# Kernel tuning notes

Hardware: AMD Instinct MI355X
Metric: run time of the kernel (lower is better)

Reference implementation:

```python
import jax, jax.numpy as jnp
import numpy as np

HEADS = 4; C = 128; D = C // HEADS; L = 2
TKG_LEN = 24; NU = 2000; NL = 5000; E = 40000
B = 64; S = 128; MAX_USER = 5000; MAX_LOC = 10000


def _seg_softmax(logits, seg, num_seg):
    # per-destination-node softmax over incoming edges, per head. logits: [E, H]
    m = jax.ops.segment_max(logits, seg, num_segments=num_seg)
    e = jnp.exp(logits - m[seg])
    z = jax.ops.segment_sum(e, seg, num_segments=num_seg)
    return e / (z[seg] + 1e-16)


def _hgt_layer(xu, xl, src_ul, dst_ul, src_lu, dst_lu, wu, bu, wl, bl, ra, rm, rp, skip):
    # PyG HGTConv math. wu/wl: [4,C,C] (k,q,v,a), bu/bl: [4,C];
    # ra/rm: [2,H,D,D] per edge type (0: user->loc, 1: loc->user); rp: [2,H]; skip: [2] (user, loc)
    def kqv(x, w, b):
        return [(x @ w[i] + b[i]).reshape(-1, HEADS, D) for i in range(3)]
    ku, qu, vu = kqv(xu, wu, bu)
    kl, ql, vl = kqv(xl, wl, bl)
    scale = 1.0 / np.sqrt(D).astype(np.float32)

    def edge_msg(k_src, v_src, q_dst, src, dst, a_rel, m_rel, p_rel, n_dst):
        kr = jnp.einsum('nhd,hde->nhe', k_src, a_rel)   # relation-transformed keys
        mr = jnp.einsum('nhd,hde->nhe', v_src, m_rel)   # relation-transformed messages
        logits = (q_dst[dst] * kr[src]).sum(-1) * p_rel * scale  # [E, H]
        alpha = _seg_softmax(logits, dst, n_dst)
        return jax.ops.segment_sum(mr[src] * alpha[..., None], dst, num_segments=n_dst)  # [N,H,D]

    agg_l = edge_msg(ku, vu, ql, src_ul, dst_ul, ra[0], rm[0], rp[0], xl.shape[0])
    agg_u = edge_msg(kl, vl, qu, src_lu, dst_lu, ra[1], rm[1], rp[1], xu.shape[0])

    def update(agg, x, wa, ba, s):
        out = jax.nn.gelu(agg.reshape(-1, C), approximate=False) @ wa + ba
        g = jax.nn.sigmoid(s)
        return g * out + (1.0 - g) * x

    return (update(agg_u, xu, wu[3], bu[3], skip[0]),
            update(agg_l, xl, wl[3], bl[3], skip[1]))


def setup_inputs():
    key = jax.random.key(0)
    ks = jax.random.split(key, 20)
    w = lambda k, shape, s=0.05: jax.random.normal(k, shape, jnp.float32) * s
    user_emb = w(ks[0], (MAX_USER, C), 0.1).at[0].set(0.0)  # padding_idx=0
    loc_emb = w(ks[1], (MAX_LOC, C), 0.1).at[0].set(0.0)
    return dict(
        user_emb=user_emb, loc_emb=loc_emb,
        lin_user_w=w(ks[2], (C, C)), lin_user_b=jnp.zeros((C,), jnp.float32),
        lin_loc_w=w(ks[3], (C, C)), lin_loc_b=jnp.zeros((C,), jnp.float32),
        w_user=w(ks[4], (L, 4, C, C)), b_user=jnp.zeros((L, 4, C), jnp.float32),
        w_loc=w(ks[5], (L, 4, C, C)), b_loc=jnp.zeros((L, 4, C), jnp.float32),
        rel_a=w(ks[6], (L, 2, HEADS, D, D), 1.0 / np.sqrt(D)),
        rel_m=w(ks[7], (L, 2, HEADS, D, D), 1.0 / np.sqrt(D)),
        rel_p=jnp.ones((L, 2, HEADS), jnp.float32),
        skip=jnp.ones((L, 2), jnp.float32),
        lin2_w=w(ks[8], (C, C)), lin2_b=jnp.zeros((C,), jnp.float32),
        user_ids=jax.random.randint(ks[9], (TKG_LEN, NU), 0, MAX_USER),
        loc_ids=jax.random.randint(ks[10], (TKG_LEN, NL), 0, MAX_LOC),
        ei_ul_src=jax.random.randint(ks[11], (TKG_LEN, E), 0, NU),
        ei_ul_dst=jax.random.randint(ks[12], (TKG_LEN, E), 0, NL),
        ei_lu_src=jax.random.randint(ks[13], (TKG_LEN, E), 0, NL),
        ei_lu_dst=jax.random.randint(ks[14], (TKG_LEN, E), 0, NU),
        traj=jax.random.randint(ks[15], (B, S), 0, NL),
        tkg_idx=jax.random.randint(ks[16], (B, S), 0, TKG_LEN),
    )


def reference(user_emb, loc_emb, lin_user_w, lin_user_b, lin_loc_w, lin_loc_b,
              w_user, b_user, w_loc, b_loc, rel_a, rel_m, rel_p, skip,
              lin2_w, lin2_b, user_ids, loc_ids, ei_ul_src, ei_ul_dst,
              ei_lu_src, ei_lu_dst, traj, tkg_idx):
    def encode(uid, lid, sul, dul, slu, dlu):
        # EmbeddingLayer lookup + AggregationLayer: per-node-type Linear + relu, HGT convs, lin2 on locations
        xu = jax.nn.relu(user_emb[uid] @ lin_user_w + lin_user_b)
        xl = jax.nn.relu(loc_emb[lid] @ lin_loc_w + lin_loc_b)
        for i in range(L):
            xu, xl = _hgt_layer(xu, xl, sul, dul, slu, dlu,
                                w_user[i], b_user[i], w_loc[i], b_loc[i],
                                rel_a[i], rel_m[i], rel_p[i], skip[i])
        return xl @ lin2_w + lin2_b

    # the torch loop over tkg_dl snapshots -> vmap over the tkg_len axis
    tkg_out = jax.vmap(encode)(user_ids, loc_ids, ei_ul_src, ei_ul_dst, ei_lu_src, ei_lu_dst)
    # tkg_filter: one-hot mask multiply-sum == direct gather tkg_out[tkg_idx[b,s], traj[b,s]]
    tkg_traj = tkg_out[tkg_idx, traj]  # [B, S, C]
    return (tkg_traj, tkg_out)
```

## Files before the change

kernel.cpp:

```cpp
#include <hip/hip_runtime.h>
#include <math.h>

#define T_LEN 24
#define NUU 2000
#define NLL 5000
#define NE 40000
#define CH 128
#define NH 4
#define HD 32
#define TCHUNK 8

typedef __attribute__((ext_vector_type(8))) short short8;
typedef __attribute__((ext_vector_type(4))) float f32x4;

static inline int cdiv(int a, int b) { return (a + b - 1) / b; }

__device__ __forceinline__ unsigned short f2bf(float x) {
    unsigned u = __float_as_uint(x);
    unsigned r = (u + 0x7fff + ((u >> 16) & 1)) >> 16;
    return (unsigned short)r;
}
__device__ __forceinline__ float bf2f(unsigned short h) {
    return __uint_as_float(((unsigned)h) << 16);
}
__device__ __forceinline__ float2 bf2x(unsigned u) {
    float2 r;
    r.x = __uint_as_float(u << 16);
    r.y = __uint_as_float(u & 0xffff0000u);
    return r;
}

__global__ void fill_zero_int(int* __restrict__ p, int n) {
    int i = blockIdx.x * blockDim.x + threadIdx.x;
    if (i < n) p[i] = 0;
}

__global__ void histo_kernel(const int* __restrict__ dst, int* __restrict__ deg, int n) {
    int idx = blockIdx.x * blockDim.x + threadIdx.x;
    if (idx >= T_LEN * NE) return;
    int t = idx / NE;
    atomicAdd(&deg[t * n + dst[idx]], 1);
}

__global__ __launch_bounds__(256) void scan_off(const int* __restrict__ deg, int* __restrict__ offo, int n) {
    __shared__ int part[256];
    int t = blockIdx.x, tid = threadIdx.x;
    int items = (n + 255) / 256;
    int start = tid * items, end = min(start + items, n);
    const int* dt = deg + t * n;
    int s = 0;
    for (int i = start; i < end; ++i) s += dt[i];
    part[tid] = s;
    __syncthreads();
    for (int d = 1; d < 256; d <<= 1) {
        int v = (tid >= d) ? part[tid - d] : 0;
        __syncthreads();
        part[tid] += v;
        __syncthreads();
    }
    int run = part[tid] - s;
    int* ot = offo + t * (n + 1);
    if (tid == 0) ot[0] = 0;
    for (int i = start; i < end; ++i) { run += dt[i]; ot[i + 1] = run; }
}

__global__ void copy_cur(const int* __restrict__ offo, int* __restrict__ cur, int n) {
    int idx = blockIdx.x * blockDim.x + threadIdx.x;
    if (idx >= T_LEN * n) return;
    int t = idx / n, i = idx - t * n;
    cur[idx] = offo[t * (n + 1) + i];
}

__global__ void scatter_perm(const int* __restrict__ dst, int* __restrict__ cur,
                             int* __restrict__ perm, int n) {
    int idx = blockIdx.x * blockDim.x + threadIdx.x;
    if (idx >= T_LEN * NE) return;
    int t = idx / NE, e = idx - t * NE;
    int d = dst[idx];
    int pos = atomicAdd(&cur[t * n + d], 1);
    perm[t * NE + pos] = e;
}

__global__ void src_sorted_k(const int* __restrict__ src, const int* __restrict__ perm,
                             int* __restrict__ out) {
    int idx = blockIdx.x * blockDim.x + threadIdx.x;
    if (idx >= T_LEN * NE) return;
    int t = idx / NE;
    out[idx] = src[(size_t)t * NE + perm[idx]];
}

__global__ __launch_bounds__(256) void build_fused(
    const float* __restrict__ w, const float* __restrict__ b,
    const float* __restrict__ ra, const float* __restrict__ rm,
    float* __restrict__ Wf, float* __restrict__ bf) {
    int idx = blockIdx.x * 256 + threadIdx.x;
    if (idx >= 128 * 384) return;
    int c = idx / 384, col = idx - c * 384;
    if (col < 128) {
        Wf[c * 384 + col] = w[16384 + c * 128 + col];
        if (c == 0) bf[col] = b[128 + col];
    } else {
        int sec = (col - 128) >> 7;
        int hc = (col - 128) & 127;
        int h = hc >> 5, e2 = hc & 31;
        const float* A = (sec == 0 ? ra : rm) + h * 1024;
        const float* wsrc = w + (sec == 0 ? 0 : 2) * 16384;
        const float* bsrc = b + (sec == 0 ? 0 : 2) * 128;
        float s = 0.f, sb = 0.f;
#pragma unroll
        for (int d = 0; d < 32; ++d) {
            float a = A[d * 32 + e2];
            s += wsrc[c * 128 + h * 32 + d] * a;
            sb += bsrc[h * 32 + d] * a;
        }
        Wf[c * 384 + col] = s;
        if (c == 0) bf[col] = sb;
    }
}

__global__ void bprep_kernel(const float* __restrict__ W, unsigned short* __restrict__ prep, int N) {
    int idx = blockIdx.x * blockDim.x + threadIdx.x;
    if (idx >= 128 * N) return;
    int k = idx / N, n = idx - k * N;
    float v = W[idx];
    unsigned short hi = f2bf(v);
    unsigned short lo = f2bf(v - bf2f(hi));
    int nt = n >> 6, nl = n & 63;
    size_t base = (size_t)nt * 16384 + (size_t)nl * 128 + k;
    prep[base] = hi;
    prep[base + 8192] = lo;
}

template <bool GATHER, int EPI>
__global__ __launch_bounds__(256) void gemm_mfma(
    const float* __restrict__ A, const int* __restrict__ ids,
    const unsigned short* __restrict__ prep, const float* __restrict__ bias,
    float* __restrict__ C, const float* __restrict__ Xold,
    const float* __restrict__ skipPtr, unsigned short* __restrict__ km,
    int M, int NC) {
    __shared__ __align__(16) char smem[65536];

    const int tid = threadIdx.x;
    const int lane = tid & 63;
    const int wid = tid >> 6;
    const int wm = wid >> 1, wn = wid & 1;
    const int m0 = blockIdx.x * 128;
    const int n0 = blockIdx.y * 64;
    const int l15 = lane & 15, l4 = lane >> 4;

    const unsigned short* bp = prep + (size_t)blockIdx.y * 16384;
    short8 bh[2][4], bl[2][4];
#pragma unroll
    for (int nf = 0; nf < 2; ++nf) {
        int ncol = wn * 32 + nf * 16 + l15;
#pragma unroll
        for (int ks = 0; ks < 4; ++ks) {
            size_t off = (size_t)ncol * 128 + ks * 32 + l4 * 8;
            bh[nf][ks] = *(const short8*)(bp + off);
            bl[nf][ks] = *(const short8*)(bp + 8192 + off);
        }
    }

#pragma unroll
    for (int i = 0; i < 16; ++i) {
        int flat = i * 256 + tid;
        int r = flat >> 5, c4 = flat & 31;
        int gr = m0 + r;
        if (gr >= M) gr = M - 1;
        int arow = GATHER ? ids[gr] : gr;
        float4 v = *(const float4*)(A + (size_t)arow * 128 + c4 * 4);
        unsigned short h0 = f2bf(v.x), h1 = f2bf(v.y), h2 = f2bf(v.z), h3 = f2bf(v.w);
        unsigned short q0 = f2bf(v.x - bf2f(h0)), q1 = f2bf(v.y - bf2f(h1));
        unsigned short q2 = f2bf(v.z - bf2f(h2)), q3 = f2bf(v.w - bf2f(h3));
        uint2 hp, lp;
        hp.x = (unsigned)h0 | ((unsigned)h1 << 16);
        hp.y = (unsigned)h2 | ((unsigned)h3 << 16);
        lp.x = (unsigned)q0 | ((unsigned)q1 << 16);
        lp.y = (unsigned)q2 | ((unsigned)q3 << 16);
        int off = r * 256 + ((c4 * 8) ^ ((r & 7) << 4));
        *(uint2*)(smem + off) = hp;
        *(uint2*)(smem + 32768 + off) = lp;
    }
    __syncthreads();

    f32x4 acc[4][2];
#pragma unroll
    for (int m = 0; m < 4; ++m)
#pragma unroll
        for (int nf = 0; nf < 2; ++nf) acc[m][nf] = (f32x4)0.f;

#pragma unroll
    for (int ks = 0; ks < 4; ++ks) {
        short8 ah[4], al[4];
#pragma unroll
        for (int m = 0; m < 4; ++m) {
            int row = wm * 64 + m * 16 + l15;
            int off = row * 256 + ((ks * 64 + l4 * 16) ^ ((row & 7) << 4));
            ah[m] = *(const short8*)(smem + off);
            al[m] = *(const short8*)(smem + 32768 + off);
        }
#pragma unroll
        for (int m = 0; m < 4; ++m)
#pragma unroll
            for (int nf = 0; nf < 2; ++nf) {
                acc[m][nf] = __builtin_amdgcn_mfma_f32_16x16x32_bf16(al[m], bh[nf][ks], acc[m][nf], 0, 0, 0);
                acc[m][nf] = __builtin_amdgcn_mfma_f32_16x16x32_bf16(ah[m], bl[nf][ks], acc[m][nf], 0, 0, 0);
                acc[m][nf] = __builtin_amdgcn_mfma_f32_16x16x32_bf16(ah[m], bh[nf][ks], acc[m][nf], 0, 0, 0);
            }
    }

    float g = 0.f;
    if (EPI == 2) g = 1.f / (1.f + expf(-skipPtr[0]));
    float bias_v[2];
#pragma unroll
    for (int nf = 0; nf < 2; ++nf) bias_v[nf] = bias[n0 + wn * 32 + nf * 16 + l15];

#pragma unroll
    for (int m = 0; m < 4; ++m) {
#pragma unroll
        for (int nf = 0; nf < 2; ++nf) {
            int gc = n0 + wn * 32 + nf * 16 + l15;
#pragma unroll
            for (int i = 0; i < 4; ++i) {
                int gr = m0 + wm * 64 + m * 16 + l4 * 4 + i;
                if (gr >= M) continue;
                float x = acc[m][nf][i] + bias_v[nf];
                if (EPI == 1) x = fmaxf(x, 0.f);
                if (EPI == 2) {
                    float xo = Xold[(size_t)gr * NC + gc];
                    x = g * x + (1.f - g) * xo;
                }
                if (EPI == 3) {
                    if (gc < 128) C[(size_t)gr * 128 + gc] = x;
                    else km[(size_t)gr * 256 + (gc - 128)] = f2bf(x);
                } else {
                    C[(size_t)gr * NC + gc] = x;
                }
            }
        }
    }
}

__global__ __launch_bounds__(256) void agg_edges(
    const float* __restrict__ qD,
    const unsigned short* __restrict__ kmS,
    const int* __restrict__ off,
    const int* __restrict__ ssrc,
    const float* __restrict__ relp,
    float* __restrict__ agg,
    int nDst, int nSrc, int tBase) {
    int idx = blockIdx.x * 256 + threadIdx.x;
    int total = TCHUNK * nDst * NH * 4;
    if (idx >= total) return;
    int h = idx & 3;
    int slot = (idx >> 2) & 3;
    int node = (idx >> 4) % nDst;
    int tl = (idx >> 4) / nDst;
    int t = tBase + tl;

    size_t drow = (size_t)(tl * nDst + node);
    float p = relp[h] * 0.17677669529663687f;

    const float4* qp = (const float4*)(qD + drow * 128 + h * HD);
    float qr[HD];
#pragma unroll
    for (int j = 0; j < 8; j++) {
        float4 v = qp[j];
        qr[4 * j + 0] = v.x * p; qr[4 * j + 1] = v.y * p;
        qr[4 * j + 2] = v.z * p; qr[4 * j + 3] = v.w * p;
    }

    float m = -INFINITY, z = 0.f;
    float acc[HD];
#pragma unroll
    for (int d = 0; d < HD; d++) acc[d] = 0.f;

    int e0 = off[t * (nDst + 1) + node], e1 = off[t * (nDst + 1) + node + 1];
    const int* ssT = ssrc + (size_t)t * NE;

    for (int i = e0 + slot; i < e1; i += 4) {
        int s = ssT[i];
        const uint4* kp = (const uint4*)(kmS + ((size_t)(tl * nSrc + s)) * 256);
        uint ku[16], mu_[16];
        *(uint4*)(ku + 0) = kp[h * 4 + 0];
        *(uint4*)(ku + 4) = kp[h * 4 + 1];
        *(uint4*)(ku + 8) = kp[h * 4 + 2];
        *(uint4*)(ku + 12) = kp[h * 4 + 3];
        *(uint4*)(mu_ + 0) = kp[16 + h * 4 + 0];
        *(uint4*)(mu_ + 4) = kp[16 + h * 4 + 1];
        *(uint4*)(mu_ + 8) = kp[16 + h * 4 + 2];
        *(uint4*)(mu_ + 12) = kp[16 + h * 4 + 3];

        float dot = 0.f;
#pragma unroll
        for (int j = 0; j < 16; ++j) {
            float2 f = bf2x(ku[j]);
            dot = fmaf(qr[2 * j], f.x, dot);
            dot = fmaf(qr[2 * j + 1], f.y, dot);
        }
        float mn = fmaxf(m, dot);
        float c = __expf(m - mn);
        float w = __expf(dot - mn);
        z = z * c + w;
#pragma unroll
        for (int j = 0; j < 16; ++j) {
            float2 f = bf2x(mu_[j]);
            acc[2 * j] = fmaf(w, f.x, acc[2 * j] * c);
            acc[2 * j + 1] = fmaf(w, f.y, acc[2 * j + 1] * c);
        }
        m = mn;
    }

#pragma unroll
    for (int lm = 4; lm <= 8; lm <<= 1) {
        float mo = __shfl_xor(m, lm);
        float zo = __shfl_xor(z, lm);
        float mn = fmaxf(m, mo);
        float s1 = (m > -INFINITY) ? __expf(m - mn) : 0.f;
        float s2 = (mo > -INFINITY) ? __expf(mo - mn) : 0.f;
        z = z * s1 + zo * s2;
#pragma unroll
        for (int d = 0; d < HD; d++) {
            float ao = __shfl_xor(acc[d], lm);
            acc[d] = acc[d] * s1 + ao * s2;
        }
        m = mn;
    }

    if (slot == 0) {
        float inv = 1.f / (z + 1e-16f);
        float* op = agg + drow * CH + h * HD;
#pragma unroll
        for (int d = 0; d < HD; d++) {
            float v = acc[d] * inv;
            v = 0.5f * v * (1.f + erff(v * 0.70710678118654752f));
            op[d] = v;
        }
    }
}

__global__ void gather_traj(const float* __restrict__ tkg, const int* __restrict__ traj,
                            const int* __restrict__ tki, float* __restrict__ outp) {
    int idx = blockIdx.x * blockDim.x + threadIdx.x;
    if (idx >= 64 * 128 * 128) return;
    int r = idx >> 7, c2 = idx & 127;
    int t = tki[r], n = traj[r];
    outp[idx] = tkg[((size_t)t * NLL + n) * CH + c2];
}

extern "C" void kernel_launch(void* const* d_in, const int* in_sizes, int n_in,
                              void* d_out, int out_size, void* d_ws, size_t ws_size,
                              hipStream_t stream) {
    (void)in_sizes; (void)n_in; (void)out_size; (void)ws_size;
    const float* user_emb = (const float*)d_in[0];
    const float* loc_emb = (const float*)d_in[1];
    const float* lin_user_w = (const float*)d_in[2];
    const float* lin_user_b = (const float*)d_in[3];
    const float* lin_loc_w = (const float*)d_in[4];
    const float* lin_loc_b = (const float*)d_in[5];
    const float* w_user = (const float*)d_in[6];
    const float* b_user = (const float*)d_in[7];
    const float* w_loc = (const float*)d_in[8];
    const float* b_loc = (const float*)d_in[9];
    const float* rel_a = (const float*)d_in[10];
    const float* rel_m = (const float*)d_in[11];
    const float* rel_p = (const float*)d_in[12];
    const float* skip = (const float*)d_in[13];
    const float* lin2_w = (const float*)d_in[14];
    const float* lin2_b = (const float*)d_in[15];
    const int* user_ids = (const int*)d_in[16];
    const int* loc_ids = (const int*)d_in[17];
    const int* ei_ul_src = (const int*)d_in[18];
    const int* ei_ul_dst = (const int*)d_in[19];
    const int* ei_lu_src = (const int*)d_in[20];
    const int* ei_lu_dst = (const int*)d_in[21];
    const int* traj = (const int*)d_in[22];
    const int* tkg_idx = (const int*)d_in[23];
    float* outp = (float*)d_out;

    size_t woff = 0;
    char* base = (char*)d_ws;
    auto carve = [&](size_t bytes) -> void* {
        void* p = base + woff;
        woff += (bytes + 255) & ~(size_t)255;
        return p;
    };
    float* xu = (float*)carve((size_t)T_LEN * NUU * 128 * 4);
    float* xl = (float*)carve((size_t)T_LEN * NLL * 128 * 4);
    float* q_u = (float*)carve((size_t)TCHUNK * NUU * 128 * 4);
    float* q_l = (float*)carve((size_t)TCHUNK * NLL * 128 * 4);
    unsigned short* km_u = (unsigned short*)carve((size_t)TCHUNK * NUU * 256 * 2);
    unsigned short* km_l = (unsigned short*)carve((size_t)TCHUNK * NLL * 256 * 2);
    float* agg_u = (float*)carve((size_t)TCHUNK * NUU * 128 * 4);
    float* agg_l = (float*)carve((size_t)TCHUNK * NLL * 128 * 4);
    float* wf_u = (float*)carve(128 * 384 * 4);
    float* bf_u = (float*)carve(384 * 4);
    float* wf_l = (float*)carve(128 * 384 * 4);
    float* bf_l = (float*)carve(384 * 4);
    int* deg_ul = (int*)carve((size_t)T_LEN * NLL * 4);
    int* cur_ul = (int*)carve((size_t)T_LEN * NLL * 4);
    int* off_ul = (int*)carve((size_t)T_LEN * (NLL + 1) * 4);
    int* perm_ul = (int*)carve((size_t)T_LEN * NE * 4);
    int* ss_ul = (int*)carve((size_t)T_LEN * NE * 4);
    int* deg_lu = (int*)carve((size_t)T_LEN * NUU * 4);
    int* cur_lu = (int*)carve((size_t)T_LEN * NUU * 4);
    int* off_lu = (int*)carve((size_t)T_LEN * (NUU + 1) * 4);
    int* perm_lu = (int*)carve((size_t)T_LEN * NE * 4);
    int* ss_lu = (int*)carve((size_t)T_LEN * NE * 4);
    unsigned short* bp_lin_u = (unsigned short*)carve(128 * 512);
    unsigned short* bp_lin_l = (unsigned short*)carve(128 * 512);
    unsigned short* bp_lin2 = (unsigned short*)carve(128 * 512);
    unsigned short* bp_upd_u[2] = {(unsigned short*)carve(128 * 512), (unsigned short*)carve(128 * 512)};
    unsigned short* bp_upd_l[2] = {(unsigned short*)carve(128 * 512), (unsigned short*)carve(128 * 512)};
    unsigned short* bp_wf_u = (unsigned short*)carve(384 * 512);
    unsigned short* bp_wf_l = (unsigned short*)carve(384 * 512);

    fill_zero_int<<<cdiv(T_LEN * NLL, 256), 256, 0, stream>>>(deg_ul, T_LEN * NLL);
    fill_zero_int<<<cdiv(T_LEN * NUU, 256), 256, 0, stream>>>(deg_lu, T_LEN * NUU);
    histo_kernel<<<cdiv(T_LEN * NE, 256), 256, 0, stream>>>(ei_ul_dst, deg_ul, NLL);
    histo_kernel<<<cdiv(T_LEN * NE, 256), 256, 0, stream>>>(ei_lu_dst, deg_lu, NUU);
    scan_off<<<T_LEN, 256, 0, stream>>>(deg_ul, off_ul, NLL);
    scan_off<<<T_LEN, 256, 0, stream>>>(deg_lu, off_lu, NUU);
    copy_cur<<<cdiv(T_LEN * NLL, 256), 256, 0, stream>>>(off_ul, cur_ul, NLL);
    copy_cur<<<cdiv(T_LEN * NUU, 256), 256, 0, stream>>>(off_lu, cur_lu, NUU);
    scatter_perm<<<cdiv(T_LEN * NE, 256), 256, 0, stream>>>(ei_ul_dst, cur_ul, perm_ul, NLL);
    scatter_perm<<<cdiv(T_LEN * NE, 256), 256, 0, stream>>>(ei_lu_dst, cur_lu, perm_lu, NUU);
    src_sorted_k<<<cdiv(T_LEN * NE, 256), 256, 0, stream>>>(ei_ul_src, perm_ul, ss_ul);
    src_sorted_k<<<cdiv(T_LEN * NE, 256), 256, 0, stream>>>(ei_lu_src, perm_lu, ss_lu);

    bprep_kernel<<<64, 256, 0, stream>>>(lin_user_w, bp_lin_u, 128);
    bprep_kernel<<<64, 256, 0, stream>>>(lin_loc_w, bp_lin_l, 128);
    bprep_kernel<<<64, 256, 0, stream>>>(lin2_w, bp_lin2, 128);
    for (int l = 0; l < 2; ++l) {
        bprep_kernel<<<64, 256, 0, stream>>>(w_user + (size_t)(l * 4 + 3) * 16384, bp_upd_u[l], 128);
        bprep_kernel<<<64, 256, 0, stream>>>(w_loc + (size_t)(l * 4 + 3) * 16384, bp_upd_l[l], 128);
    }

    gemm_mfma<true, 1><<<dim3(cdiv(T_LEN * NUU, 128), 2), 256, 0, stream>>>(
        user_emb, user_ids, bp_lin_u, lin_user_b, xu, nullptr, nullptr, nullptr, T_LEN * NUU, 128);
    gemm_mfma<true, 1><<<dim3(cdiv(T_LEN * NLL, 128), 2), 256, 0, stream>>>(
        loc_emb, loc_ids, bp_lin_l, lin_loc_b, xl, nullptr, nullptr, nullptr, T_LEN * NLL, 128);

    for (int l = 0; l < 2; ++l) {
        build_fused<<<cdiv(128 * 384, 256), 256, 0, stream>>>(
            w_user + (size_t)l * 4 * 16384, b_user + l * 512,
            rel_a + (size_t)(l * 2 + 0) * 4096, rel_m + (size_t)(l * 2 + 0) * 4096, wf_u, bf_u);
        build_fused<<<cdiv(128 * 384, 256), 256, 0, stream>>>(
            w_loc + (size_t)l * 4 * 16384, b_loc + l * 512,
            rel_a + (size_t)(l * 2 + 1) * 4096, rel_m + (size_t)(l * 2 + 1) * 4096, wf_l, bf_l);
        bprep_kernel<<<192, 256, 0, stream>>>(wf_u, bp_wf_u, 384);
        bprep_kernel<<<192, 256, 0, stream>>>(wf_l, bp_wf_l, 384);

        for (int tb = 0; tb < T_LEN; tb += TCHUNK) {
            const int MU = TCHUNK * NUU;
            const int ML = TCHUNK * NLL;
            float* xu_c = xu + (size_t)tb * NUU * 128;
            float* xl_c = xl + (size_t)tb * NLL * 128;

            gemm_mfma<false, 3><<<dim3(cdiv(MU, 128), 6), 256, 0, stream>>>(
                xu_c, nullptr, bp_wf_u, bf_u, q_u, nullptr, nullptr, km_u, MU, 384);
            gemm_mfma<false, 3><<<dim3(cdiv(ML, 128), 6), 256, 0, stream>>>(
                xl_c, nullptr, bp_wf_l, bf_l, q_l, nullptr, nullptr, km_l, ML, 384);

            agg_edges<<<cdiv(TCHUNK * NLL * NH * 4, 256), 256, 0, stream>>>(
                q_l, km_u, off_ul, ss_ul, rel_p + (l * 2 + 0) * 4, agg_l, NLL, NUU, tb);
            agg_edges<<<cdiv(TCHUNK * NUU * NH * 4, 256), 256, 0, stream>>>(
                q_u, km_l, off_lu, ss_lu, rel_p + (l * 2 + 1) * 4, agg_u, NUU, NLL, tb);

            gemm_mfma<false, 2><<<dim3(cdiv(MU, 128), 2), 256, 0, stream>>>(
                agg_u, nullptr, bp_upd_u[l], b_user + l * 512 + 384,
                xu_c, xu_c, skip + l * 2 + 0, nullptr, MU, 128);
            gemm_mfma<false, 2><<<dim3(cdiv(ML, 128), 2), 256, 0, stream>>>(
                agg_l, nullptr, bp_upd_l[l], b_loc + l * 512 + 384,
                xl_c, xl_c, skip + l * 2 + 1, nullptr, ML, 128);
        }
    }

    float* tkg_out = outp + (size_t)64 * 128 * 128;
    gemm_mfma<false, 0><<<dim3(cdiv(T_LEN * NLL, 128), 2), 256, 0, stream>>>(
        xl, nullptr, bp_lin2, lin2_b, tkg_out, nullptr, nullptr, nullptr, T_LEN * NLL, 128);

    gather_traj<<<cdiv(64 * 128 * 128, 256), 256, 0, stream>>>(tkg_out, traj, tkg_idx, outp);
}
```

Measured before the change: 1.636 ms.

## Fuse CSR build kernels, remap GEMM workgroups per XCD, widen edge slots

Merges copy_cur into scan_off and fuses the scatter_perm and src_sorted kernels into one scatter_src that writes source ids straight into CSR order, which drops several launches and the perm buffers. The MFMA GEMM now remaps its flat workgroup id so that consecutive tiles land on the same XCD, aimed at better L2 locality across the chiplets. agg_edges uses 8 edge slots per (node, head) instead of 4, with one more shuffle-reduction step, to add parallelism for high-degree nodes. The cost is more threads doing reductions and extra integer math at GEMM entry; the order of edges within a segment is still nondeterministic.

```diff
diff --git a/kernel.cpp b/kernel.cpp
--- a/kernel.cpp
+++ b/kernel.cpp
@@ -42,7 +42,8 @@
     atomicAdd(&deg[t * n + dst[idx]], 1);
 }
 
-__global__ __launch_bounds__(256) void scan_off(const int* __restrict__ deg, int* __restrict__ offo, int n) {
+__global__ __launch_bounds__(256) void scan_off(const int* __restrict__ deg, int* __restrict__ offo,
+                                                int* __restrict__ cur, int n) {
     __shared__ int part[256];
     int t = blockIdx.x, tid = threadIdx.x;
     int items = (n + 255) / 256;
@@ -60,33 +61,23 @@
     }
     int run = part[tid] - s;
     int* ot = offo + t * (n + 1);
+    int* ct = cur + t * n;
     if (tid == 0) ot[0] = 0;
-    for (int i = start; i < end; ++i) { run += dt[i]; ot[i + 1] = run; }
-}
-
-__global__ void copy_cur(const int* __restrict__ offo, int* __restrict__ cur, int n) {
-    int idx = blockIdx.x * blockDim.x + threadIdx.x;
-    if (idx >= T_LEN * n) return;
-    int t = idx / n, i = idx - t * n;
-    cur[idx] = offo[t * (n + 1) + i];
-}
-
-__global__ void scatter_perm(const int* __restrict__ dst, int* __restrict__ cur,
-                             int* __restrict__ perm, int n) {
-    int idx = blockIdx.x * blockDim.x + threadIdx.x;
-    if (idx >= T_LEN * NE) return;
-    int t = idx / NE, e = idx - t * NE;
-    int d = dst[idx];
-    int pos = atomicAdd(&cur[t * n + d], 1);
-    perm[t * NE + pos] = e;
-}
-
-__global__ void src_sorted_k(const int* __restrict__ src, const int* __restrict__ perm,
-                             int* __restrict__ out) {
+    for (int i = start; i < end; ++i) {
+        ct[i] = run;
+        run += dt[i];
+        ot[i + 1] = run;
+    }
+}
+
+__global__ void scatter_src(const int* __restrict__ dst, const int* __restrict__ src,
+                            int* __restrict__ cur, int* __restrict__ ssrc, int n) {
     int idx = blockIdx.x * blockDim.x + threadIdx.x;
     if (idx >= T_LEN * NE) return;
     int t = idx / NE;
-    out[idx] = src[(size_t)t * NE + perm[idx]];
+    int d = dst[idx];
+    int pos = atomicAdd(&cur[t * n + d], 1);
+    ssrc[(size_t)t * NE + pos] = src[idx];
 }
 
 __global__ __launch_bounds__(256) void build_fused(
@@ -142,13 +133,20 @@
 
     const int tid = threadIdx.x;
     const int lane = tid & 63;
-    const int wid = tid >> 6;
-    const int wm = wid >> 1, wn = wid & 1;
-    const int m0 = blockIdx.x * 128;
-    const int n0 = blockIdx.y * 64;
+    const int wid_w = tid >> 6;
+    const int wm = wid_w >> 1, wn = wid_w & 1;
     const int l15 = lane & 15, l4 = lane >> 4;
 
-    const unsigned short* bp = prep + (size_t)blockIdx.y * 16384;
+    const int nx = gridDim.x, ny = gridDim.y;
+    int flat = blockIdx.y * nx + blockIdx.x;
+    int nwg = nx * ny;
+    int q = nwg >> 3, r = nwg & 7;
+    int xcd = flat & 7, rank = flat >> 3;
+    int wgid = (xcd < r ? xcd * (q + 1) : r * (q + 1) + (xcd - r) * q) + rank;
+    const int m0 = (wgid / ny) * 128;
+    const int n0 = (wgid % ny) * 64;
+
+    const unsigned short* bp = prep + (size_t)(wgid % ny) * 16384;
     short8 bh[2][4], bl[2][4];
 #pragma unroll
     for (int nf = 0; nf < 2; ++nf) {
@@ -163,9 +161,9 @@
 
 #pragma unroll
     for (int i = 0; i < 16; ++i) {
-        int flat = i * 256 + tid;
-        int r = flat >> 5, c4 = flat & 31;
-        int gr = m0 + r;
+        int flat2 = i * 256 + tid;
+        int rr = flat2 >> 5, c4 = flat2 & 31;
+        int gr = m0 + rr;
         if (gr >= M) gr = M - 1;
         int arow = GATHER ? ids[gr] : gr;
         float4 v = *(const float4*)(A + (size_t)arow * 128 + c4 * 4);
@@ -177,7 +175,7 @@
         hp.y = (unsigned)h2 | ((unsigned)h3 << 16);
         lp.x = (unsigned)q0 | ((unsigned)q1 << 16);
         lp.y = (unsigned)q2 | ((unsigned)q3 << 16);
-        int off = r * 256 + ((c4 * 8) ^ ((r & 7) << 4));
+        int off = rr * 256 + ((c4 * 8) ^ ((rr & 7) << 4));
         *(uint2*)(smem + off) = hp;
         *(uint2*)(smem + 32768 + off) = lp;
     }
@@ -250,12 +248,12 @@
     float* __restrict__ agg,
     int nDst, int nSrc, int tBase) {
     int idx = blockIdx.x * 256 + threadIdx.x;
-    int total = TCHUNK * nDst * NH * 4;
+    int total = TCHUNK * nDst * NH * 8;
     if (idx >= total) return;
     int h = idx & 3;
-    int slot = (idx >> 2) & 3;
-    int node = (idx >> 4) % nDst;
-    int tl = (idx >> 4) / nDst;
+    int slot = (idx >> 2) & 7;
+    int node = (idx >> 5) % nDst;
+    int tl = (idx >> 5) / nDst;
     int t = tBase + tl;
 
     size_t drow = (size_t)(tl * nDst + node);
@@ -278,7 +276,7 @@
     int e0 = off[t * (nDst + 1) + node], e1 = off[t * (nDst + 1) + node + 1];
     const int* ssT = ssrc + (size_t)t * NE;
 
-    for (int i = e0 + slot; i < e1; i += 4) {
+    for (int i = e0 + slot; i < e1; i += 8) {
         int s = ssT[i];
         const uint4* kp = (const uint4*)(kmS + ((size_t)(tl * nSrc + s)) * 256);
         uint ku[16], mu_[16];
@@ -312,7 +310,7 @@
     }
 
 #pragma unroll
-    for (int lm = 4; lm <= 8; lm <<= 1) {
+    for (int lm = 4; lm <= 16; lm <<= 1) {
         float mo = __shfl_xor(m, lm);
         float zo = __shfl_xor(z, lm);
         float mn = fmaxf(m, mo);
@@ -400,12 +398,10 @@
     int* deg_ul = (int*)carve((size_t)T_LEN * NLL * 4);
     int* cur_ul = (int*)carve((size_t)T_LEN * NLL * 4);
     int* off_ul = (int*)carve((size_t)T_LEN * (NLL + 1) * 4);
-    int* perm_ul = (int*)carve((size_t)T_LEN * NE * 4);
     int* ss_ul = (int*)carve((size_t)T_LEN * NE * 4);
     int* deg_lu = (int*)carve((size_t)T_LEN * NUU * 4);
     int* cur_lu = (int*)carve((size_t)T_LEN * NUU * 4);
     int* off_lu = (int*)carve((size_t)T_LEN * (NUU + 1) * 4);
-    int* perm_lu = (int*)carve((size_t)T_LEN * NE * 4);
     int* ss_lu = (int*)carve((size_t)T_LEN * NE * 4);
     unsigned short* bp_lin_u = (unsigned short*)carve(128 * 512);
     unsigned short* bp_lin_l = (unsigned short*)carve(128 * 512);
@@ -419,14 +415,10 @@
     fill_zero_int<<<cdiv(T_LEN * NUU, 256), 256, 0, stream>>>(deg_lu, T_LEN * NUU);
     histo_kernel<<<cdiv(T_LEN * NE, 256), 256, 0, stream>>>(ei_ul_dst, deg_ul, NLL);
     histo_kernel<<<cdiv(T_LEN * NE, 256), 256, 0, stream>>>(ei_lu_dst, deg_lu, NUU);
-    scan_off<<<T_LEN, 256, 0, stream>>>(deg_ul, off_ul, NLL);
-    scan_off<<<T_LEN, 256, 0, stream>>>(deg_lu, off_lu, NUU);
-    copy_cur<<<cdiv(T_LEN * NLL, 256), 256, 0, stream>>>(off_ul, cur_ul, NLL);
-    copy_cur<<<cdiv(T_LEN * NUU, 256), 256, 0, stream>>>(off_lu, cur_lu, NUU);
-    scatter_perm<<<cdiv(T_LEN * NE, 256), 256, 0, stream>>>(ei_ul_dst, cur_ul, perm_ul, NLL);
-    scatter_perm<<<cdiv(T_LEN * NE, 256), 256, 0, stream>>>(ei_lu_dst, cur_lu, perm_lu, NUU);
-    src_sorted_k<<<cdiv(T_LEN * NE, 256), 256, 0, stream>>>(ei_ul_src, perm_ul, ss_ul);
-    src_sorted_k<<<cdiv(T_LEN * NE, 256), 256, 0, stream>>>(ei_lu_src, perm_lu, ss_lu);
+    scan_off<<<T_LEN, 256, 0, stream>>>(deg_ul, off_ul, cur_ul, NLL);
+    scan_off<<<T_LEN, 256, 0, stream>>>(deg_lu, off_lu, cur_lu, NUU);
+    scatter_src<<<cdiv(T_LEN * NE, 256), 256, 0, stream>>>(ei_ul_dst, ei_ul_src, cur_ul, ss_ul, NLL);
+    scatter_src<<<cdiv(T_LEN * NE, 256), 256, 0, stream>>>(ei_lu_dst, ei_lu_src, cur_lu, ss_lu, NUU);
 
     bprep_kernel<<<64, 256, 0, stream>>>(lin_user_w, bp_lin_u, 128);
     bprep_kernel<<<64, 256, 0, stream>>>(lin_loc_w, bp_lin_l, 128);
@@ -462,9 +454,9 @@
             gemm_mfma<false, 3><<<dim3(cdiv(ML, 128), 6), 256, 0, stream>>>(
                 xl_c, nullptr, bp_wf_l, bf_l, q_l, nullptr, nullptr, km_l, ML, 384);
 
-            agg_edges<<<cdiv(TCHUNK * NLL * NH * 4, 256), 256, 0, stream>>>(
+            agg_edges<<<cdiv(TCHUNK * NLL * NH * 8, 256), 256, 0, stream>>>(
                 q_l, km_u, off_ul, ss_ul, rel_p + (l * 2 + 0) * 4, agg_l, NLL, NUU, tb);
-            agg_edges<<<cdiv(TCHUNK * NUU * NH * 4, 256), 256, 0, stream>>>(
+            agg_edges<<<cdiv(TCHUNK * NUU * NH * 8, 256), 256, 0, stream>>>(
                 q_u, km_l, off_lu, ss_lu, rel_p + (l * 2 + 1) * 4, agg_u, NUU, NLL, tb);
 
             gemm_mfma<false, 2><<<dim3(cdiv(MU, 128), 2), 256, 0, stream>>>(
```

After: 1.659 ms. About the same (+1.4%).
